# Performance work log

Hardware: AMD Instinct MI355X
Metric: run time of the kernel (lower is better)

Reference implementation:

```python
import jax, jax.numpy as jnp
import numpy as np

N, E, D, H, C = 50000, 800000, 128, 128, 40
EPS = 1e-5


def setup_inputs() -> dict:
    key = jax.random.key(0)
    ks = jax.random.split(key, 18)
    s = lambda d: 1.0 / np.sqrt(d)
    inp = {
        "x": jax.random.normal(ks[0], (N, D), dtype=jnp.float32),
        "edge_index": jax.random.randint(ks[1], (2, E), 0, N, dtype=jnp.int64),
        # GCNConv weights (x @ W + b after normalized aggregation)
        "W1": jax.random.normal(ks[2], (D, H), dtype=jnp.float32) * s(D),
        "b1": jax.random.normal(ks[3], (H,), dtype=jnp.float32) * 0.01,
        "W2": jax.random.normal(ks[4], (H, H), dtype=jnp.float32) * s(H),
        "b2": jax.random.normal(ks[5], (H,), dtype=jnp.float32) * 0.01,
        "W3": jax.random.normal(ks[6], (H, H), dtype=jnp.float32) * s(H),
        "b3": jax.random.normal(ks[7], (H,), dtype=jnp.float32) * 0.01,
        # LayerNorm params (applied after layers 0 and 1 only)
        "ln1_g": 1.0 + 0.1 * jax.random.normal(ks[8], (H,), dtype=jnp.float32),
        "ln1_b": 0.1 * jax.random.normal(ks[9], (H,), dtype=jnp.float32),
        "ln2_g": 1.0 + 0.1 * jax.random.normal(ks[10], (H,), dtype=jnp.float32),
        "ln2_b": 0.1 * jax.random.normal(ks[11], (H,), dtype=jnp.float32),
        # post_mp MLP head
        "mpW1": jax.random.normal(ks[12], (H, H), dtype=jnp.float32) * s(H),
        "mpb1": jax.random.normal(ks[13], (H,), dtype=jnp.float32) * 0.01,
        "mpW2": jax.random.normal(ks[14], (H, C), dtype=jnp.float32) * s(H),
        "mpb2": jax.random.normal(ks[15], (C,), dtype=jnp.float32) * 0.01,
    }
    return inp


def _layernorm(h, g, b):
    mu = jnp.mean(h, axis=-1, keepdims=True)
    var = jnp.mean((h - mu) ** 2, axis=-1, keepdims=True)
    return (h - mu) * jax.lax.rsqrt(var + EPS) * g + b


def _gcn_forward(x, edge_index, params):
    (W1, b1, W2, b2, W3, b3, ln1_g, ln1_b, ln2_g, ln2_b, mpW1, mpb1, mpW2, mpb2) = params
    n = x.shape[0]
    loop = jnp.arange(n, dtype=edge_index.dtype)
    src = jnp.concatenate([edge_index[0], loop])  # source-to-target flow + self-loops
    dst = jnp.concatenate([edge_index[1], loop])
    deg = jax.ops.segment_sum(jnp.ones_like(src, dtype=x.dtype), dst, num_segments=n)
    dis = jax.lax.rsqrt(deg)  # deg >= 1 due to self-loops
    norm = dis[src] * dis[dst]  # [E+N]

    def conv(h, W, b):
        h = h @ W
        msg = h[src] * norm[:, None]  # gather + scale
        return jax.ops.segment_sum(msg, dst, num_segments=n) + b  # scatter-add

    h = x
    # layer 0
    h = conv(h, W1, b1)
    h = jax.nn.relu(h)  # dropout p=0.1 -> identity in eval
    h = _layernorm(h, ln1_g, ln1_b)
    # layer 1
    h = conv(h, W2, b2)
    h = jax.nn.relu(h)
    h = _layernorm(h, ln2_g, ln2_b)
    # layer 2 (emb is pre-relu conv output)
    emb = conv(h, W3, b3)
    h = jax.nn.relu(emb)
    # post_mp: Linear -> Dropout(eval: identity) -> Linear
    h = h @ mpW1 + mpb1
    logits = h @ mpW2 + mpb2
    return emb, jax.nn.log_softmax(logits, axis=1)


def reference(x, edge_index, W1, b1, W2, b2, W3, b3, ln1_g, ln1_b, ln2_g, ln2_b, mpW1, mpb1, mpW2, mpb2):
    params = (W1, b1, W2, b2, W3, b3, ln1_g, ln1_b, ln2_g, ln2_b, mpW1, mpb1, mpW2, mpb2)
    return _gcn_forward(x, edge_index, params)
```

## Files before the change

kernel.cpp:

```cpp
#include <hip/hip_runtime.h>

typedef __bf16 bf16x8 __attribute__((ext_vector_type(8)));
typedef float  f32x4  __attribute__((ext_vector_type(4)));
typedef float  f32x2  __attribute__((ext_vector_type(2)));
typedef unsigned short u16;
typedef unsigned int   u32;
typedef long long      i64;

#define BSH  7
#define BCAP 4096
#define NPB  256

__device__ __forceinline__ float b2f(u16 x){ return __uint_as_float(((u32)x) << 16); }
__device__ __forceinline__ u16 f2b(float x){
  u32 u = __float_as_uint(x);
  return (u16)((u + 0x7FFFu + ((u >> 16) & 1u)) >> 16);
}

__device__ __forceinline__ void d2acc(u32 pair, f32x2& a){
  f32x2 t;
  t.x = __uint_as_float(pair << 16);
  t.y = __uint_as_float(pair & 0xFFFF0000u);
  a += t;
}
__device__ __forceinline__ void acc8(uint4 q, f32x2* a){
  d2acc(q.x, a[0]); d2acc(q.y, a[1]); d2acc(q.z, a[2]); d2acc(q.w, a[3]);
}

__global__ __launch_bounds__(256) void k_detect(const u16* __restrict__ x,
                                                const u32* __restrict__ ei,
                                                int* __restrict__ flags){
  __shared__ int sh[2];
  int t = threadIdx.x;
  if (t < 2) sh[t] = 0;
  __syncthreads();
  int sane = 0;
  for (int i = t; i < 4096; i += 256){
    u16 u = x[i]; u32 e = (u >> 7) & 0xFFu;
    if (u == 0 || (e >= 0x70u && e <= 0x8Fu)) sane++;
  }
  int nz = 0;
  for (int i = t; i < 1024; i += 256)
    if (ei[2*i + 1] != 0u) nz++;
  atomicAdd(&sh[0], sane);
  atomicAdd(&sh[1], nz);
  __syncthreads();
  if (t == 0){
    flags[0] = (sh[0] < 3500) ? 1 : 0;
    flags[1] = (sh[1] == 0) ? 1 : 0;
  }
}

__device__ __forceinline__ int ld_idx(const void* ei, long long j, int is64){
  return is64 ? (int)((const i64*)ei)[j] : ((const int*)ei)[j];
}
__device__ __forceinline__ void ld8(const void* p, int base, int f, float* o){
  if (f){
    float4 a = *(const float4*)((const float*)p + base);
    float4 b = *(const float4*)((const float*)p + base + 4);
    o[0]=a.x; o[1]=a.y; o[2]=a.z; o[3]=a.w;
    o[4]=b.x; o[5]=b.y; o[6]=b.z; o[7]=b.w;
  } else {
    uint4 q = *(const uint4*)((const u16*)p + base);
    o[0]=b2f((u16)(q.x&0xffff)); o[1]=b2f((u16)(q.x>>16));
    o[2]=b2f((u16)(q.y&0xffff)); o[3]=b2f((u16)(q.y>>16));
    o[4]=b2f((u16)(q.z&0xffff)); o[5]=b2f((u16)(q.z>>16));
    o[6]=b2f((u16)(q.w&0xffff)); o[7]=b2f((u16)(q.w>>16));
  }
}

__global__ __launch_bounds__(256) void k_partA(const void* __restrict__ ei, int E, int n,
                                               int* __restrict__ cntmat,
                                               const int* __restrict__ flags, int nbuk){
  __shared__ int cnt[512];
  int t = threadIdx.x;
  int is64 = flags[1];
  for (int i = t; i < 512; i += 256) cnt[i] = 0;
  __syncthreads();
  long long R = ((long long)E + NPB - 1) / NPB;
  long long lo = (long long)blockIdx.x * R;
  long long hi = lo + R; if (hi > E) hi = E;
  for (long long e = lo + t; e < hi; e += 256){
    int d = ld_idx(ei, (long long)E + e, is64);
    if ((unsigned)d < (unsigned)n) atomicAdd(&cnt[(unsigned)d >> BSH], 1);
  }
  __syncthreads();
  for (int b = t; b < nbuk; b += 256)
    cntmat[(size_t)b*NPB + blockIdx.x] = cnt[b];
}

__global__ __launch_bounds__(NPB) void k_scanBK(const int* __restrict__ cntmat,
                                                int* __restrict__ basemat,
                                                int* __restrict__ bcnt){
  __shared__ int sh[NPB];
  int b = blockIdx.x, t = threadIdx.x;
  int v = cntmat[(size_t)b*NPB + t];
  sh[t] = v; __syncthreads();
  for (int off = 1; off < NPB; off <<= 1){
    int u = 0; if (t >= off) u = sh[t - off];
    __syncthreads(); sh[t] += u; __syncthreads();
  }
  basemat[(size_t)b*NPB + t] = sh[t] - v;
  if (t == NPB-1) bcnt[b] = sh[t];
}

__global__ __launch_bounds__(256) void k_partC(const void* __restrict__ ei, int E, int n,
                                               const int* __restrict__ basemat,
                                               u32* __restrict__ ebuf,
                                               const int* __restrict__ flags, int nbuk){
  __shared__ int cur[512];
  int t = threadIdx.x;
  int is64 = flags[1];
  for (int i = t; i < 512; i += 256) cur[i] = 0;
  __syncthreads();
  for (int b = t; b < nbuk; b += 256) cur[b] = basemat[(size_t)b*NPB + blockIdx.x];
  __syncthreads();
  long long R = ((long long)E + NPB - 1) / NPB;
  long long lo = (long long)blockIdx.x * R;
  long long hi = lo + R; if (hi > E) hi = E;
  for (long long e = lo + t; e < hi; e += 256){
    int d = ld_idx(ei, (long long)E + e, is64);
    int s = ld_idx(ei, e, is64);
    if ((unsigned)d < (unsigned)n && (unsigned)s < (unsigned)n){
      int b = (unsigned)d >> BSH;
      int p = atomicAdd(&cur[b], 1);
      if (p < BCAP) ebuf[(size_t)b*BCAP + p] = (u32)s | ((u32)(d & ((1<<BSH)-1)) << 17);
    }
  }
}

__global__ __launch_bounds__(256) void k_bdeg(const int* __restrict__ bcnt,
                                              const u32* __restrict__ ebuf,
                                              int* __restrict__ deg, int n){
  __shared__ int cnt[1<<BSH];
  int b = blockIdx.x, t = threadIdx.x;
  if (t < (1<<BSH)) cnt[t] = 0;
  __syncthreads();
  int m = bcnt[b]; if (m > BCAP) m = BCAP;
  const u32* eb = ebuf + (size_t)b*BCAP;
  for (int i = t; i < m; i += 256)
    atomicAdd(&cnt[eb[i] >> 17], 1);
  __syncthreads();
  if (t < (1<<BSH)){
    int node = (b << BSH) + t;
    if (node < n) deg[node] = cnt[t];
  }
}

__global__ __launch_bounds__(256) void k_scanA(const int* __restrict__ deg, int n,
                                               int* __restrict__ bsum){
  __shared__ int sh[256];
  int t = threadIdx.x;
  int base = blockIdx.x*1024 + t*4;
  int s = 0;
  #pragma unroll
  for (int i = 0; i < 4; ++i){ int idx = base + i; if (idx < n) s += deg[idx]; }
  sh[t] = s; __syncthreads();
  for (int off = 128; off; off >>= 1){
    if (t < off) sh[t] += sh[t + off];
    __syncthreads();
  }
  if (t == 0) bsum[blockIdx.x] = sh[0];
}

__global__ __launch_bounds__(256) void k_scanB(int* __restrict__ bsum, int nB,
                                               int* __restrict__ rowptr, int n){
  __shared__ int sh[256];
  int t = threadIdx.x;
  int v = (t < nB) ? bsum[t] : 0;
  sh[t] = v; __syncthreads();
  for (int off = 1; off < 256; off <<= 1){
    int u = 0; if (t >= off) u = sh[t - off];
    __syncthreads(); sh[t] += u; __syncthreads();
  }
  if (t < nB) bsum[t] = sh[t] - v;
  if (t == 255) rowptr[n] = sh[255];
}

__global__ __launch_bounds__(256) void k_scanC(const int* __restrict__ deg, int n,
                                               const int* __restrict__ bsum,
                                               int* __restrict__ rowptr,
                                               float* __restrict__ dis){
  __shared__ int sh[256];
  int t = threadIdx.x;
  int base = blockIdx.x*1024 + t*4;
  int d[4]; int s = 0;
  #pragma unroll
  for (int i = 0; i < 4; ++i){ int idx = base + i; d[i] = (idx < n) ? deg[idx] : 0; s += d[i]; }
  sh[t] = s; __syncthreads();
  for (int off = 1; off < 256; off <<= 1){
    int u = 0; if (t >= off) u = sh[t - off];
    __syncthreads(); sh[t] += u; __syncthreads();
  }
  int run = bsum[blockIdx.x] + sh[t] - s;
  #pragma unroll
  for (int i = 0; i < 4; ++i){
    int idx = base + i;
    if (idx < n){
      rowptr[idx] = run; run += d[i];
      dis[idx] = rsqrtf((float)(d[i] + 1));
    }
  }
}

__global__ __launch_bounds__(256) void k_bfill(const int* __restrict__ bcnt,
                                               const u32* __restrict__ ebuf,
                                               const int* __restrict__ rowptr,
                                               int* __restrict__ colx, int n){
  __shared__ int cur[1<<BSH];
  int b = blockIdx.x, t = threadIdx.x;
  if (t < (1<<BSH)){
    int node = (b << BSH) + t;
    cur[t] = (node < n) ? rowptr[node] : 0;
  }
  __syncthreads();
  int m = bcnt[b]; if (m > BCAP) m = BCAP;
  const u32* eb = ebuf + (size_t)b*BCAP;
  for (int i = t; i < m; i += 256){
    u32 e = eb[i];
    int p = atomicAdd(&cur[e >> 17], 1);
    colx[p] = (int)((e & 0x1FFFFu) << 8);
  }
}

__global__ __launch_bounds__(64) void k_shufW(const void* __restrict__ W, u16* __restrict__ Ws,
                                              const int* __restrict__ flags){
  int f = flags[0];
  int bid = blockIdx.x;
  int nt = bid >> 2, kk = bid & 3;
  int l = threadIdx.x;
  int g = l >> 4, mr = l & 15;
  int nn = nt*16 + mr;
  #pragma unroll
  for (int i = 0; i < 8; ++i){
    int k = kk*32 + g*4 + (i & 3) + ((i >> 2) << 4);
    u16 w = f ? f2b(((const float*)W)[k*128 + nn]) : ((const u16*)W)[k*128 + nn];
    Ws[(size_t)(bid*64 + l)*8 + i] = w;
  }
}

__global__ __launch_bounds__(256) void k_gemm(const void* __restrict__ A, int aExt,
    const u16* __restrict__ Ws, const float* __restrict__ dis,
    u16* __restrict__ T, int nTiles, const int* __restrict__ flags)
{
  int wave = threadIdx.x >> 6, lane = threadIdx.x & 63;
  int tile = blockIdx.x*4 + wave;
  if (tile >= nTiles) return;
  int g = lane >> 4, mr = lane & 15;
  int f = aExt ? flags[0] : 0;
  union U8 { ushort4 q[2]; u16 s[8]; bf16x8 b; };
  bf16x8 a[4];
  if (f){
    const float* ap = (const float*)A + (size_t)(tile*16 + mr)*128;
    #pragma unroll
    for (int kk = 0; kk < 4; ++kk){
      float4 p = *(const float4*)(ap + kk*32 + g*4);
      float4 q = *(const float4*)(ap + kk*32 + g*4 + 16);
      U8 u;
      u.s[0]=f2b(p.x); u.s[1]=f2b(p.y); u.s[2]=f2b(p.z); u.s[3]=f2b(p.w);
      u.s[4]=f2b(q.x); u.s[5]=f2b(q.y); u.s[6]=f2b(q.z); u.s[7]=f2b(q.w);
      a[kk] = u.b;
    }
  } else {
    const u16* ap = (const u16*)A + (size_t)(tile*16 + mr)*128;
    #pragma unroll
    for (int kk = 0; kk < 4; ++kk){
      U8 u;
      u.q[0] = *(const ushort4*)(ap + kk*32 + g*4);
      u.q[1] = *(const ushort4*)(ap + kk*32 + g*4 + 16);
      a[kk] = u.b;
    }
  }
  float dj[4];
  #pragma unroll
  for (int j = 0; j < 4; ++j) dj[j] = dis[tile*16 + g*4 + j];
  #pragma unroll
  for (int nt = 0; nt < 8; ++nt){
    f32x4 acc = {0.f,0.f,0.f,0.f};
    #pragma unroll
    for (int kk = 0; kk < 4; ++kk){
      bf16x8 b = *(const bf16x8*)(Ws + (size_t)((nt*4 + kk)*64 + lane)*8);
      acc = __builtin_amdgcn_mfma_f32_16x16x32_bf16(a[kk], b, acc, 0, 0, 0);
    }
    int nn = nt*16 + mr;
    #pragma unroll
    for (int j = 0; j < 4; ++j){
      int row = tile*16 + g*4 + j;
      T[(size_t)row*128 + nn] = f2b(acc[j] * dj[j]);
    }
  }
}

template<int MODE>
__global__ __launch_bounds__(256) void k_agg(const u16* __restrict__ T,
    const int* __restrict__ rowptr, const int* __restrict__ colx,
    const float* __restrict__ dis, const void* __restrict__ bias,
    const void* __restrict__ lg, const void* __restrict__ lb,
    void* __restrict__ outA, int n, const int* __restrict__ flags)
{
  int wave = threadIdx.x >> 6, l = threadIdx.x & 63;
  int g = l >> 4, c = l & 15;
  int v = blockIdx.x*16 + wave*4 + g;
  bool alive = v < n;
  int vv = alive ? v : (n - 1);
  int f = flags[0];
  const char* Tb = (const char*)T + c*16;

  f32x2 aA[4] = {};
  f32x2 aB[4] = {};
  {
    uint4 q = *(const uint4*)(Tb + ((size_t)vv << 8));
    acc8(q, aA);
  }
  int s = rowptr[vv], e = rowptr[vv+1];
  int i = s;
  for (; i + 4 <= e; i += 4){
    int o0 = colx[i];
    int o1 = colx[i+1];
    int o2 = colx[i+2];
    int o3 = colx[i+3];
    uint4 q0 = *(const uint4*)(Tb + o0);
    uint4 q1 = *(const uint4*)(Tb + o1);
    uint4 q2 = *(const uint4*)(Tb + o2);
    uint4 q3 = *(const uint4*)(Tb + o3);
    acc8(q0, aA); acc8(q1, aB); acc8(q2, aA); acc8(q3, aB);
  }
  for (; i < e; ++i){
    uint4 q = *(const uint4*)(Tb + colx[i]);
    acc8(q, aA);
  }

  float acc[8];
  #pragma unroll
  for (int k = 0; k < 4; ++k){
    acc[2*k]   = aA[k].x + aB[k].x;
    acc[2*k+1] = aA[k].y + aB[k].y;
  }
  float sc = dis[vv];
  float bv[8]; ld8(bias, c*8, f, bv);
  float x[8];
  #pragma unroll
  for (int k = 0; k < 8; ++k) x[k] = fmaf(acc[k], sc, bv[k]);

  if (MODE == 0){
    #pragma unroll
    for (int k = 0; k < 8; ++k) x[k] = fmaxf(x[k], 0.f);
    float sum = 0.f;
    #pragma unroll
    for (int k = 0; k < 8; ++k) sum += x[k];
    #pragma unroll
    for (int off = 8; off; off >>= 1) sum += __shfl_xor(sum, off);
    float mu = sum * (1.f/128.f);
    float vs = 0.f;
    #pragma unroll
    for (int k = 0; k < 8; ++k){ float d = x[k] - mu; vs += d*d; }
    #pragma unroll
    for (int off = 8; off; off >>= 1) vs += __shfl_xor(vs, off);
    float inv = rsqrtf(vs*(1.f/128.f) + 1e-5f);
    float gv[8], bvv[8];
    ld8(lg, c*8, f, gv); ld8(lb, c*8, f, bvv);
    if (alive){
      uint4 w;
      float y0,y1;
      y0 = (x[0]-mu)*inv*gv[0] + bvv[0]; y1 = (x[1]-mu)*inv*gv[1] + bvv[1];
      w.x = (u32)f2b(y0) | ((u32)f2b(y1) << 16);
      y0 = (x[2]-mu)*inv*gv[2] + bvv[2]; y1 = (x[3]-mu)*inv*gv[3] + bvv[3];
      w.y = (u32)f2b(y0) | ((u32)f2b(y1) << 16);
      y0 = (x[4]-mu)*inv*gv[4] + bvv[4]; y1 = (x[5]-mu)*inv*gv[5] + bvv[5];
      w.z = (u32)f2b(y0) | ((u32)f2b(y1) << 16);
      y0 = (x[6]-mu)*inv*gv[6] + bvv[6]; y1 = (x[7]-mu)*inv*gv[7] + bvv[7];
      w.w = (u32)f2b(y0) | ((u32)f2b(y1) << 16);
      *(uint4*)((u16*)outA + (size_t)v*128 + c*8) = w;
    }
  } else {
    if (alive){
      if (f){
        float* oa = (float*)outA + (size_t)v*128 + c*8;
        *(float4*)(oa)     = make_float4(x[0], x[1], x[2], x[3]);
        *(float4*)(oa + 4) = make_float4(x[4], x[5], x[6], x[7]);
      } else {
        uint4 w;
        w.x = (u32)f2b(x[0]) | ((u32)f2b(x[1]) << 16);
        w.y = (u32)f2b(x[2]) | ((u32)f2b(x[3]) << 16);
        w.z = (u32)f2b(x[4]) | ((u32)f2b(x[5]) << 16);
        w.w = (u32)f2b(x[6]) | ((u32)f2b(x[7]) << 16);
        *(uint4*)((u16*)outA + (size_t)v*128 + c*8) = w;
      }
    }
  }
}

__global__ __launch_bounds__(128) void k_wc(const void* __restrict__ mpW1, const void* __restrict__ mpb1,
    const void* __restrict__ mpW2, const void* __restrict__ mpb2,
    float* __restrict__ Wc, float* __restrict__ bc, const int* __restrict__ flags)
{
  int f = flags[0];
  int c = blockIdx.x;
  int k = threadIdx.x;
  float acc = 0.f;
  if (f){
    const float* A  = (const float*)mpW1 + (size_t)k*128;
    const float* B2 = (const float*)mpW2;
    #pragma unroll 8
    for (int j = 0; j < 128; ++j) acc = fmaf(A[j], B2[j*40 + c], acc);
    if (k == 0){
      const float* b1p = (const float*)mpb1;
      float b = ((const float*)mpb2)[c];
      #pragma unroll 8
      for (int j = 0; j < 128; ++j) b = fmaf(b1p[j], B2[j*40 + c], b);
      bc[c] = b;
    }
  } else {
    const u16* A  = (const u16*)mpW1 + (size_t)k*128;
    const u16* B2 = (const u16*)mpW2;
    #pragma unroll 8
    for (int j = 0; j < 128; ++j) acc = fmaf(b2f(A[j]), b2f(B2[j*40 + c]), acc);
    if (k == 0){
      const u16* b1p = (const u16*)mpb1;
      float b = b2f(((const u16*)mpb2)[c]);
      #pragma unroll 8
      for (int j = 0; j < 128; ++j) b = fmaf(b2f(b1p[j]), b2f(B2[j*40 + c]), b);
      bc[c] = b;
    }
  }
  Wc[k*40 + c] = acc;
}

__global__ __launch_bounds__(64) void k_shufWc(const float* __restrict__ Wc, u16* __restrict__ Wcs){
  int bid = blockIdx.x;
  int nt = bid >> 2, kk = bid & 3;
  int l = threadIdx.x;
  int g = l >> 4, mr = l & 15;
  int nn = nt*16 + mr;
  #pragma unroll
  for (int i = 0; i < 8; ++i){
    int k = kk*32 + g*4 + (i & 3) + ((i >> 2) << 4);
    Wcs[(size_t)(bid*64 + l)*8 + i] = (nn < 40) ? f2b(Wc[k*40 + nn]) : (u16)0;
  }
}

__global__ __launch_bounds__(256) void k_logitsM(const u16* __restrict__ Wcs,
    const float* __restrict__ bc, void* __restrict__ dout, int n,
    const int* __restrict__ flags)
{
  int wave = threadIdx.x >> 6, lane = threadIdx.x & 63;
  int tile = blockIdx.x*4 + wave;
  int nTiles = n >> 4;
  if (tile >= nTiles) return;
  int f = flags[0];
  int g = lane >> 4, mr = lane & 15;
  union U8 { ushort4 q[2]; u16 s[8]; bf16x8 b; };
  bf16x8 a[4];
  if (f){
    const float* ap = (const float*)dout + (size_t)(tile*16 + mr)*128;
    #pragma unroll
    for (int kk = 0; kk < 4; ++kk){
      float4 p = *(const float4*)(ap + kk*32 + g*4);
      float4 q = *(const float4*)(ap + kk*32 + g*4 + 16);
      U8 u;
      u.s[0]=f2b(fmaxf(p.x,0.f)); u.s[1]=f2b(fmaxf(p.y,0.f));
      u.s[2]=f2b(fmaxf(p.z,0.f)); u.s[3]=f2b(fmaxf(p.w,0.f));
      u.s[4]=f2b(fmaxf(q.x,0.f)); u.s[5]=f2b(fmaxf(q.y,0.f));
      u.s[6]=f2b(fmaxf(q.z,0.f)); u.s[7]=f2b(fmaxf(q.w,0.f));
      a[kk] = u.b;
    }
  } else {
    const u16* ap = (const u16*)dout + (size_t)(tile*16 + mr)*128;
    #pragma unroll
    for (int kk = 0; kk < 4; ++kk){
      U8 u;
      u.q[0] = *(const ushort4*)(ap + kk*32 + g*4);
      u.q[1] = *(const ushort4*)(ap + kk*32 + g*4 + 16);
      #pragma unroll
      for (int i = 0; i < 8; ++i) u.s[i] = (u.s[i] & 0x8000u) ? (u16)0 : u.s[i];
      a[kk] = u.b;
    }
  }
  f32x4 acc[3];
  #pragma unroll
  for (int nt = 0; nt < 3; ++nt){
    f32x4 c4 = {0.f,0.f,0.f,0.f};
    #pragma unroll
    for (int kk = 0; kk < 4; ++kk){
      bf16x8 b = *(const bf16x8*)(Wcs + (size_t)((nt*4 + kk)*64 + lane)*8);
      c4 = __builtin_amdgcn_mfma_f32_16x16x32_bf16(a[kk], b, c4, 0, 0, 0);
    }
    acc[nt] = c4;
  }
  float bcv[3]; bool valid[3];
  #pragma unroll
  for (int nt = 0; nt < 3; ++nt){
    int c = nt*16 + mr;
    valid[nt] = (c < 40);
    bcv[nt] = valid[nt] ? bc[c] : 0.f;
  }
  float* of = (float*)dout + (size_t)n*128;
  u16*  ob = (u16*) dout + (size_t)n*128;
  #pragma unroll
  for (int j = 0; j < 4; ++j){
    float l0 = valid[0] ? acc[0][j] + bcv[0] : -3.0e38f;
    float l1 = valid[1] ? acc[1][j] + bcv[1] : -3.0e38f;
    float l2 = valid[2] ? acc[2][j] + bcv[2] : -3.0e38f;
    float m = fmaxf(l0, fmaxf(l1, l2));
    #pragma unroll
    for (int off = 8; off; off >>= 1) m = fmaxf(m, __shfl_xor(m, off));
    float ssum = (valid[0] ? expf(l0 - m) : 0.f)
               + (valid[1] ? expf(l1 - m) : 0.f)
               + (valid[2] ? expf(l2 - m) : 0.f);
    #pragma unroll
    for (int off = 8; off; off >>= 1) ssum += __shfl_xor(ssum, off);
    float lgs = m + logf(ssum);
    int node = tile*16 + g*4 + j;
    #pragma unroll
    for (int nt = 0; nt < 3; ++nt){
      if (valid[nt]){
        int c = nt*16 + mr;
        float r = (nt==0 ? l0 : (nt==1 ? l1 : l2)) - lgs;
        if (f) of[(size_t)node*40 + c] = r;
        else   ob[(size_t)node*40 + c] = f2b(r);
      }
    }
  }
}

extern "C" void kernel_launch(void* const* d_in, const int* in_sizes, int n_in,
                              void* d_out, int out_size, void* d_ws, size_t ws_size,
                              hipStream_t stream)
{
  const int n = in_sizes[0] / 128;
  const int E = in_sizes[1] / 2;

  const void* x    = d_in[0];
  const void* ei   = d_in[1];
  const void* W1   = d_in[2];
  const void* b1   = d_in[3];
  const void* W2   = d_in[4];
  const void* b2   = d_in[5];
  const void* W3   = d_in[6];
  const void* b3   = d_in[7];
  const void* ln1g = d_in[8];
  const void* ln1b = d_in[9];
  const void* ln2g = d_in[10];
  const void* ln2b = d_in[11];
  const void* mpW1 = d_in[12];
  const void* mpb1 = d_in[13];
  const void* mpW2 = d_in[14];
  const void* mpb2 = d_in[15];

  u16* Hbuf = (u16*)d_out;

  char* w = (char*)d_ws;
  size_t off = 0;
  auto alloc = [&](size_t bytes)->char*{
    char* p = w + off; off = (off + bytes + 255) & ~(size_t)255; return p;
  };
  const int nbuk = (n + (1<<BSH) - 1) >> BSH;

  int*   flags = (int*)  alloc(256);
  float* dis   = (float*)alloc((size_t)n*4);
  int*   deg   = (int*)  alloc((size_t)n*4);
  int*   rowp  = (int*)  alloc((size_t)(n+1)*4);
  int*   bsum  = (int*)  alloc(1024);
  int*   bcnt  = (int*)  alloc((size_t)nbuk*4);
  int*   cntm  = (int*)  alloc((size_t)nbuk*NPB*4);
  int*   basem = (int*)  alloc((size_t)nbuk*NPB*4);
  u32*   ebuf  = (u32*)  alloc((size_t)nbuk*BCAP*4);
  int*   colx  = (int*)  alloc((size_t)E*4 + 256);
  u16*   T     = (u16*)  alloc((size_t)n*128*2);
  u16*   Ws    = (u16*)  alloc((size_t)128*128*2);
  float* Wc    = (float*)alloc((size_t)128*40*4);
  float* bc    = (float*)alloc((size_t)64*4);
  u16*   Wcs   = (u16*)  alloc((size_t)12*64*8*2);

  int nB = (n + 1023) / 1024;

  k_detect<<<1, 256, 0, stream>>>((const u16*)x, (const u32*)ei, flags);
  k_partA <<<NPB, 256, 0, stream>>>(ei, E, n, cntm, flags, nbuk);
  k_scanBK<<<nbuk, NPB, 0, stream>>>(cntm, basem, bcnt);
  k_partC <<<NPB, 256, 0, stream>>>(ei, E, n, basem, ebuf, flags, nbuk);
  k_bdeg  <<<nbuk, 256, 0, stream>>>(bcnt, ebuf, deg, n);
  k_scanA <<<nB, 256, 0, stream>>>(deg, n, bsum);
  k_scanB <<<1, 256, 0, stream>>>(bsum, nB, rowp, n);
  k_scanC <<<nB, 256, 0, stream>>>(deg, n, bsum, rowp, dis);
  k_bfill <<<nbuk, 256, 0, stream>>>(bcnt, ebuf, rowp, colx, n);
  k_wc    <<<40, 128, 0, stream>>>(mpW1, mpb1, mpW2, mpb2, Wc, bc, flags);
  k_shufWc<<<12, 64, 0, stream>>>(Wc, Wcs);

  int nTiles = (n + 15) / 16;
  int gG = (nTiles + 3) / 4;
  int gA = (n + 15) / 16;

  k_shufW<<<32, 64, 0, stream>>>(W1, Ws, flags);
  k_gemm <<<gG, 256, 0, stream>>>(x, 1, Ws, dis, T, nTiles, flags);
  k_agg<0><<<gA, 256, 0, stream>>>(T, rowp, colx, dis, b1, ln1g, ln1b, Hbuf, n, flags);
  k_shufW<<<32, 64, 0, stream>>>(W2, Ws, flags);
  k_gemm <<<gG, 256, 0, stream>>>(Hbuf, 0, Ws, dis, T, nTiles, flags);
  k_agg<0><<<gA, 256, 0, stream>>>(T, rowp, colx, dis, b2, ln2g, ln2b, Hbuf, n, flags);
  k_shufW<<<32, 64, 0, stream>>>(W3, Ws, flags);
  k_gemm <<<gG, 256, 0, stream>>>(Hbuf, 0, Ws, dis, T, nTiles, flags);
  k_agg<1><<<gA, 256, 0, stream>>>(T, rowp, colx, dis, b3, nullptr, nullptr, d_out, n, flags);
  k_logitsM<<<gG, 256, 0, stream>>>(Wcs, bc, d_out, n, flags);
}
```

Baseline: 226.0 us.

## Pad CSR rows to multiples of four and merge weight shuffles

Rounds each node's neighbour list up to a multiple of four and fills the padding with an index pointing at an added all-zero row in T. This lets the aggregation loop read column indices as vector loads and drop the scalar tail loop. The three per-layer weight shuffle launches are also merged into one launch at the start, writing into a triple-sized buffer. The padding adds extra gathers of the zero row and a longer colx array.

```diff
diff --git a/kernel.cpp b/kernel.cpp
--- a/kernel.cpp
+++ b/kernel.cpp
@@ -29,7 +29,8 @@
 
 __global__ __launch_bounds__(256) void k_detect(const u16* __restrict__ x,
                                                 const u32* __restrict__ ei,
-                                                int* __restrict__ flags){
+                                                int* __restrict__ flags,
+                                                u16* __restrict__ T, int n){
   __shared__ int sh[2];
   int t = threadIdx.x;
   if (t < 2) sh[t] = 0;
@@ -44,6 +45,8 @@
     if (ei[2*i + 1] != 0u) nz++;
   atomicAdd(&sh[0], sane);
   atomicAdd(&sh[1], nz);
+  if (t < 128) T[(size_t)n*128 + t] = 0;
+  else         T[(size_t)n*128 + t] = 0;
   __syncthreads();
   if (t == 0){
     flags[0] = (sh[0] < 3500) ? 1 : 0;
@@ -154,7 +157,10 @@
   int base = blockIdx.x*1024 + t*4;
   int s = 0;
   #pragma unroll
-  for (int i = 0; i < 4; ++i){ int idx = base + i; if (idx < n) s += deg[idx]; }
+  for (int i = 0; i < 4; ++i){
+    int idx = base + i;
+    if (idx < n) s += (deg[idx] + 3) & ~3;
+  }
   sh[t] = s; __syncthreads();
   for (int off = 128; off; off >>= 1){
     if (t < off) sh[t] += sh[t + off];
@@ -186,7 +192,11 @@
   int base = blockIdx.x*1024 + t*4;
   int d[4]; int s = 0;
   #pragma unroll
-  for (int i = 0; i < 4; ++i){ int idx = base + i; d[i] = (idx < n) ? deg[idx] : 0; s += d[i]; }
+  for (int i = 0; i < 4; ++i){
+    int idx = base + i;
+    d[i] = (idx < n) ? deg[idx] : 0;
+    s += (d[i] + 3) & ~3;
+  }
   sh[t] = s; __syncthreads();
   for (int off = 1; off < 256; off <<= 1){
     int u = 0; if (t >= off) u = sh[t - off];
@@ -197,7 +207,7 @@
   for (int i = 0; i < 4; ++i){
     int idx = base + i;
     if (idx < n){
-      rowptr[idx] = run; run += d[i];
+      rowptr[idx] = run; run += (d[i] + 3) & ~3;
       dis[idx] = rsqrtf((float)(d[i] + 1));
     }
   }
@@ -209,10 +219,9 @@
                                                int* __restrict__ colx, int n){
   __shared__ int cur[1<<BSH];
   int b = blockIdx.x, t = threadIdx.x;
-  if (t < (1<<BSH)){
-    int node = (b << BSH) + t;
+  int node = (b << BSH) + (t & ((1<<BSH)-1));
+  if (t < (1<<BSH))
     cur[t] = (node < n) ? rowptr[node] : 0;
-  }
   __syncthreads();
   int m = bcnt[b]; if (m > BCAP) m = BCAP;
   const u32* eb = ebuf + (size_t)b*BCAP;
@@ -221,12 +230,24 @@
     int p = atomicAdd(&cur[e >> 17], 1);
     colx[p] = (int)((e & 0x1FFFFu) << 8);
   }
-}
-
-__global__ __launch_bounds__(64) void k_shufW(const void* __restrict__ W, u16* __restrict__ Ws,
-                                              const int* __restrict__ flags){
+  __syncthreads();
+  if (t < (1<<BSH) && node < n){
+    int zoff = n << 8;
+    int end = rowptr[node + 1];
+    for (int p = cur[t]; p < end; ++p) colx[p] = zoff;
+  }
+}
+
+__global__ __launch_bounds__(64) void k_shufW3(const void* __restrict__ W1,
+                                               const void* __restrict__ W2,
+                                               const void* __restrict__ W3,
+                                               u16* __restrict__ Ws,
+                                               const int* __restrict__ flags){
   int f = flags[0];
-  int bid = blockIdx.x;
+  int sel = blockIdx.x >> 5;
+  const void* W = (sel == 0) ? W1 : (sel == 1) ? W2 : W3;
+  u16* Wo = Ws + (size_t)sel * 128 * 128;
+  int bid = blockIdx.x & 31;
   int nt = bid >> 2, kk = bid & 3;
   int l = threadIdx.x;
   int g = l >> 4, mr = l & 15;
@@ -235,7 +256,7 @@
   for (int i = 0; i < 8; ++i){
     int k = kk*32 + g*4 + (i & 3) + ((i >> 2) << 4);
     u16 w = f ? f2b(((const float*)W)[k*128 + nn]) : ((const u16*)W)[k*128 + nn];
-    Ws[(size_t)(bid*64 + l)*8 + i] = w;
+    Wo[(size_t)(bid*64 + l)*8 + i] = w;
   }
 }
 
@@ -314,20 +335,27 @@
   }
   int s = rowptr[vv], e = rowptr[vv+1];
   int i = s;
-  for (; i + 4 <= e; i += 4){
-    int o0 = colx[i];
-    int o1 = colx[i+1];
-    int o2 = colx[i+2];
-    int o3 = colx[i+3];
-    uint4 q0 = *(const uint4*)(Tb + o0);
-    uint4 q1 = *(const uint4*)(Tb + o1);
-    uint4 q2 = *(const uint4*)(Tb + o2);
-    uint4 q3 = *(const uint4*)(Tb + o3);
+  for (; i + 8 <= e; i += 8){
+    uint4 oA = *(const uint4*)(colx + i);
+    uint4 oB = *(const uint4*)(colx + i + 4);
+    uint4 q0 = *(const uint4*)(Tb + oA.x);
+    uint4 q1 = *(const uint4*)(Tb + oA.y);
+    uint4 q2 = *(const uint4*)(Tb + oA.z);
+    uint4 q3 = *(const uint4*)(Tb + oA.w);
+    uint4 q4 = *(const uint4*)(Tb + oB.x);
+    uint4 q5 = *(const uint4*)(Tb + oB.y);
+    uint4 q6 = *(const uint4*)(Tb + oB.z);
+    uint4 q7 = *(const uint4*)(Tb + oB.w);
     acc8(q0, aA); acc8(q1, aB); acc8(q2, aA); acc8(q3, aB);
-  }
-  for (; i < e; ++i){
-    uint4 q = *(const uint4*)(Tb + colx[i]);
-    acc8(q, aA);
+    acc8(q4, aA); acc8(q5, aB); acc8(q6, aA); acc8(q7, aB);
+  }
+  if (i < e){
+    uint4 o = *(const uint4*)(colx + i);
+    uint4 q0 = *(const uint4*)(Tb + o.x);
+    uint4 q1 = *(const uint4*)(Tb + o.y);
+    uint4 q2 = *(const uint4*)(Tb + o.z);
+    uint4 q3 = *(const uint4*)(Tb + o.w);
+    acc8(q0, aA); acc8(q1, aB); acc8(q2, aA); acc8(q3, aB);
   }
 
   float acc[8];
@@ -565,16 +593,17 @@
   int*   cntm  = (int*)  alloc((size_t)nbuk*NPB*4);
   int*   basem = (int*)  alloc((size_t)nbuk*NPB*4);
   u32*   ebuf  = (u32*)  alloc((size_t)nbuk*BCAP*4);
-  int*   colx  = (int*)  alloc((size_t)E*4 + 256);
-  u16*   T     = (u16*)  alloc((size_t)n*128*2);
-  u16*   Ws    = (u16*)  alloc((size_t)128*128*2);
+  int*   colx  = (int*)  alloc(((size_t)E + 4*(size_t)n)*4 + 256);
+  u16*   T     = (u16*)  alloc((size_t)(n+1)*128*2);
+  u16*   Ws    = (u16*)  alloc((size_t)3*128*128*2);
   float* Wc    = (float*)alloc((size_t)128*40*4);
   float* bc    = (float*)alloc((size_t)64*4);
   u16*   Wcs   = (u16*)  alloc((size_t)12*64*8*2);
 
   int nB = (n + 1023) / 1024;
 
-  k_detect<<<1, 256, 0, stream>>>((const u16*)x, (const u32*)ei, flags);
+  k_detect<<<1, 256, 0, stream>>>((const u16*)x, (const u32*)ei, flags, T, n);
+  k_shufW3<<<96, 64, 0, stream>>>(W1, W2, W3, Ws, flags);
   k_partA <<<NPB, 256, 0, stream>>>(ei, E, n, cntm, flags, nbuk);
   k_scanBK<<<nbuk, NPB, 0, stream>>>(cntm, basem, bcnt);
   k_partC <<<NPB, 256, 0, stream>>>(ei, E, n, basem, ebuf, flags, nbuk);
@@ -590,14 +619,11 @@
   int gG = (nTiles + 3) / 4;
   int gA = (n + 15) / 16;
 
-  k_shufW<<<32, 64, 0, stream>>>(W1, Ws, flags);
   k_gemm <<<gG, 256, 0, stream>>>(x, 1, Ws, dis, T, nTiles, flags);
   k_agg<0><<<gA, 256, 0, stream>>>(T, rowp, colx, dis, b1, ln1g, ln1b, Hbuf, n, flags);
-  k_shufW<<<32, 64, 0, stream>>>(W2, Ws, flags);
-  k_gemm <<<gG, 256, 0, stream>>>(Hbuf, 0, Ws, dis, T, nTiles, flags);
+  k_gemm <<<gG, 256, 0, stream>>>(Hbuf, 0, Ws + (size_t)128*128, dis, T, nTiles, flags);
   k_agg<0><<<gA, 256, 0, stream>>>(T, rowp, colx, dis, b2, ln2g, ln2b, Hbuf, n, flags);
-  k_shufW<<<32, 64, 0, stream>>>(W3, Ws, flags);
-  k_gemm <<<gG, 256, 0, stream>>>(Hbuf, 0, Ws, dis, T, nTiles, flags);
+  k_gemm <<<gG, 256, 0, stream>>>(Hbuf, 0, Ws + (size_t)2*128*128, dis, T, nTiles, flags);
   k_agg<1><<<gA, 256, 0, stream>>>(T, rowp, colx, dis, b3, nullptr, nullptr, d_out, n, flags);
   k_logitsM<<<gG, 256, 0, stream>>>(Wcs, bc, d_out, n, flags);
 }
```

Measured after the change: 213.3 us. -5.6%, faster.
